# Optimization experiments

Measured on AMD Instinct MI355X. Metric: run time of the kernel, lower is better.

Reference implementation:

```python
import jax, jax.numpy as jnp
import numpy as np

C, N, B = 16, 65536, 4096  # cases, points per case, batch of case IDs


def _w(key, fan_in, fan_out):
    return jax.random.normal(key, (fan_in, fan_out), dtype=jnp.float32) / np.sqrt(fan_in).astype(np.float32)


def setup_inputs() -> dict:
    key = jax.random.key(0)
    ks = jax.random.split(key, 8)
    pts = jax.random.normal(ks[0], (C, N, 3), dtype=jnp.float32)
    inp = {
        "pts": pts,
        "W1_0": _w(ks[1], 3, 64), "b1_0": jnp.zeros((64,), jnp.float32),
        "W1_1": _w(ks[2], 64, 128), "b1_1": jnp.zeros((128,), jnp.float32),
        "W1_2": _w(ks[3], 128, 512), "b1_2": jnp.zeros((512,), jnp.float32),
        "W2_0": _w(ks[4], 512, 256), "b2_0": jnp.zeros((256,), jnp.float32),
        "W2_1": _w(ks[5], 256, 512), "b2_1": jnp.zeros((512,), jnp.float32),
        "x": jax.random.randint(ks[6], (B,), 0, C, dtype=jnp.int64),
    }
    return inp


def reference(pts, W1_0, b1_0, W1_1, b1_1, W1_2, b1_2, W2_0, b2_0, W2_1, b2_1, x):
    def mlp1(h):  # shared per-point MLP, SiLU after every layer
        h = jax.nn.silu(h @ W1_0 + b1_0)
        h = jax.nn.silu(h @ W1_1 + b1_1)
        h = jax.nn.silu(h @ W1_2 + b1_2)
        return h

    feats = mlp1(pts)                       # [C, N, F1]
    idx = jnp.argmax(feats, axis=1)         # [C, F1] critical-point indices per feature
    # gather critical points (detached in the torch original)
    fixed = jax.lax.stop_gradient(pts[jnp.arange(pts.shape[0])[:, None], idx])  # [C, F1, 3]

    feats2 = mlp1(fixed)                    # [C, F1, F1]
    latent0 = jnp.max(feats2, axis=1)       # [C, F1]

    h = jax.nn.silu(latent0 @ W2_0 + b2_0)  # [C, 256]
    latent = h @ W2_1 + b2_1                # [C, total_modes*ge_features]

    caseID_unit = jax.nn.one_hot(x, latent.shape[0], dtype=latent.dtype)  # [B, C]
    return caseID_unit @ latent             # [B, 512]
```

## Files before the change

kernel.cpp:

```cpp
#include <hip/hip_runtime.h>
#include <math.h>

#define NCASES   16
#define NPTS_BIG 65536
#define OUT_B    4096

typedef __attribute__((ext_vector_type(8))) short  short8;
typedef __attribute__((ext_vector_type(4))) float  floatx4;

__device__ __forceinline__ float silu_f(float x) {
    return x * __builtin_amdgcn_rcpf(1.0f + __expf(-x));
}

__device__ __forceinline__ unsigned f2bf_hi(float x) {
    unsigned u = __float_as_uint(x);
    return u + 0x7FFFu + ((u >> 16) & 1u);
}
__device__ __forceinline__ unsigned short f2bf(float x) {
    return (unsigned short)(f2bf_hi(x) >> 16);
}
__device__ __forceinline__ unsigned pk2bf_rtz(float lo, float hi) {
    return __builtin_amdgcn_perm(__float_as_uint(hi), __float_as_uint(lo), 0x07060302u);
}

__device__ __forceinline__ unsigned enc_f(float x) {
    unsigned u = __float_as_uint(x);
    return (u & 0x80000000u) ? ~u : (u | 0x80000000u);
}

__device__ __forceinline__ float sgpr_f(float x) {
    return __uint_as_float(__builtin_amdgcn_readfirstlane(__float_as_uint(x)));
}

__global__ void k_prep(const float* __restrict__ W11, const float* __restrict__ W12,
                       unsigned short* __restrict__ BbWs, unsigned short* __restrict__ BcWs,
                       unsigned long long* __restrict__ argBuf)
{
    int i = blockIdx.x * 256 + threadIdx.x;
    if (i < 8192) argBuf[i] = 0ull;
    {
        int j = i & 7, l = (i >> 3) & 63, t = i >> 9;
        int KT = t & 3, NT = (t >> 2) & 3, w = t >> 4;
        int k = KT * 32 + (l >> 4) * 8 + j;
        int f = w * 64 + NT * 16 + (l & 15);
        BcWs[i] = f2bf(W12[(size_t)k * 512 + f]);
    }
    if (i < 8192) {
        int j = i & 7, l = (i >> 3) & 63, t = i >> 9;
        int KT = t & 1, w = t >> 1;
        int k = KT * 32 + (l >> 4) * 8 + j;
        int f = w * 16 + (l & 15);
        BbWs[i] = f2bf(W11[(size_t)k * 128 + f]);
    }
}

template<bool GATHER>
__device__ __forceinline__ void mlp1_pipeline(
    const float* __restrict__ cpts,
    const unsigned long long* __restrict__ gIdx,
    int chunk0, int nChunks,
    const float* __restrict__ W10, const float* __restrict__ b10,
    const float* __restrict__ b11,
    const unsigned short* __restrict__ BbWs,
    const unsigned short* __restrict__ BcWs,
    unsigned short* __restrict__ s_h0,
    unsigned short* __restrict__ s_h1,
    int wf, int l, int lm, int q, float* bestv)
{
    float wA0[8], wA1[8], wA2[8], bA[8];
    #pragma unroll
    for (int j = 0; j < 8; ++j) {
        wA0[j] = sgpr_f(W10[  0 + wf * 8 + j]);
        wA1[j] = sgpr_f(W10[ 64 + wf * 8 + j]);
        wA2[j] = sgpr_f(W10[128 + wf * 8 + j]);
        bA[j]  = sgpr_f(b10[       wf * 8 + j]);
    }

    short8 Bc[16];
    #pragma unroll
    for (int t = 0; t < 16; ++t)
        Bc[t] = *(const short8*)(BcWs + (size_t)((wf * 16 + t) * 64 + l) * 8);
    short8 Bb0 = *(const short8*)(BbWs + (size_t)((wf * 2 + 0) * 64 + l) * 8);
    short8 Bb1 = *(const short8*)(BbWs + (size_t)((wf * 2 + 1) * 64 + l) * 8);

    const float bias11 = b11[wf * 16 + lm];
    const floatx4 bias4 = {bias11, bias11, bias11, bias11};
    const floatx4 fzero = {0.f, 0.f, 0.f, 0.f};

    #pragma unroll
    for (int NT = 0; NT < 4; ++NT) bestv[NT] = -INFINITY;

    float ax[2], ay[2], az[2];
    {
        const int pb = chunk0 * 128;
        #pragma unroll
        for (int h = 0; h < 2; ++h) {
            const float* sp;
            if (GATHER) {
                unsigned gi = ~(unsigned)(gIdx[pb + h * 64 + l] & 0xFFFFFFFFull);
                sp = cpts + (size_t)gi * 3;
            } else {
                sp = cpts + (size_t)(pb + h * 64 + l) * 3;
            }
            ax[h] = sp[0]; ay[h] = sp[1]; az[h] = sp[2];
        }
    }

    for (int ch = 0; ch < nChunks; ++ch) {
        #pragma unroll
        for (int h = 0; h < 2; ++h) {
            float v[8];
            #pragma unroll
            for (int j = 0; j < 8; ++j) {
                float t = fmaf(az[h], wA2[j], bA[j]);
                t = fmaf(ay[h], wA1[j], t);
                t = fmaf(ax[h], wA0[j], t);
                v[j] = silu_f(t);
            }
            uint4 hv = { pk2bf_rtz(v[0], v[1]), pk2bf_rtz(v[2], v[3]),
                         pk2bf_rtz(v[4], v[5]), pk2bf_rtz(v[6], v[7]) };
            *(uint4*)&s_h0[(h * 64 + l) * 72 + wf * 8] = hv;
        }
        __syncthreads();

        if (ch + 1 < nChunks) {
            const int pb = (chunk0 + ch + 1) * 128;
            #pragma unroll
            for (int h = 0; h < 2; ++h) {
                const float* sp;
                if (GATHER) {
                    unsigned gi = ~(unsigned)(gIdx[pb + h * 64 + l] & 0xFFFFFFFFull);
                    sp = cpts + (size_t)gi * 3;
                } else {
                    sp = cpts + (size_t)(pb + h * 64 + l) * 3;
                }
                ax[h] = sp[0]; ay[h] = sp[1]; az[h] = sp[2];
            }
        }

        #pragma unroll
        for (int MT = 0; MT < 8; ++MT) {
            const unsigned short* ar = s_h0 + (MT * 16 + lm) * 72;
            short8 a0 = *(const short8*)(ar + q * 8);
            short8 a1 = *(const short8*)(ar + 32 + q * 8);
            floatx4 acc = __builtin_amdgcn_mfma_f32_16x16x32_bf16(a0, Bb0, bias4, 0, 0, 0);
            acc = __builtin_amdgcn_mfma_f32_16x16x32_bf16(a1, Bb1, acc, 0, 0, 0);
            #pragma unroll
            for (int r = 0; r < 4; ++r) {
                unsigned uv = __float_as_uint(silu_f(acc[r]));
                s_h1[(MT * 16 + q * 4 + r) * 136 + wf * 16 + lm] = (unsigned short)(uv >> 16);
            }
        }
        __syncthreads();

        #pragma unroll
        for (int MT = 0; MT < 8; ++MT) {
            const unsigned short* ar = s_h1 + (MT * 16 + lm) * 136;
            short8 a[4];
            #pragma unroll
            for (int KT = 0; KT < 4; ++KT)
                a[KT] = *(const short8*)(ar + KT * 32 + q * 8);
            const int cbM = 127 - (ch << 5) - (MT << 2);
            #pragma unroll
            for (int NT = 0; NT < 4; ++NT) {
                floatx4 acc = __builtin_amdgcn_mfma_f32_16x16x32_bf16(a[0], Bc[NT * 4], fzero, 0, 0, 0);
                #pragma unroll
                for (int KT = 1; KT < 4; ++KT)
                    acc = __builtin_amdgcn_mfma_f32_16x16x32_bf16(a[KT], Bc[NT * 4 + KT], acc, 0, 0, 0);
                float x0 = __uint_as_float((__float_as_uint(acc[0]) & 0xFFFFFF80u) | (unsigned)(cbM));
                float x1 = __uint_as_float((__float_as_uint(acc[1]) & 0xFFFFFF80u) | (unsigned)(cbM - 1));
                float x2 = __uint_as_float((__float_as_uint(acc[2]) & 0xFFFFFF80u) | (unsigned)(cbM - 2));
                float x3 = __uint_as_float((__float_as_uint(acc[3]) & 0xFFFFFF80u) | (unsigned)(cbM - 3));
                float t0 = fmaxf(fmaxf(x0, x1), x2);
                bestv[NT] = fmaxf(fmaxf(t0, x3), bestv[NT]);
            }
        }
    }
}

__global__ __launch_bounds__(512, 4)
void k_mlp1_argmax(const float* __restrict__ pts,
                   const float* __restrict__ W10, const float* __restrict__ b10,
                   const float* __restrict__ b11, const float* __restrict__ b12,
                   const unsigned short* __restrict__ BbWs,
                   const unsigned short* __restrict__ BcWs,
                   unsigned long long* __restrict__ argOut)
{
    const int c = blockIdx.y, tid = threadIdx.x;
    const int wf = __builtin_amdgcn_readfirstlane(tid >> 6);
    const int l = tid & 63, lm = l & 15, q = l >> 4;

    __shared__ __align__(16) unsigned short s_h0[128 * 72];
    __shared__ __align__(16) unsigned short s_h1[128 * 136];

    float bestv[4];
    mlp1_pipeline<false>(pts + (size_t)c * NPTS_BIG * 3, nullptr,
                         blockIdx.x * 4, 4, W10, b10, b11, BbWs, BcWs,
                         s_h0, s_h1, wf, l, lm, q, bestv);

    #pragma unroll
    for (int NT = 0; NT < 4; ++NT) {
        unsigned u = __float_as_uint(bestv[NT]);
        int t = 127 - (int)(u & 127u);
        unsigned idx = (unsigned)((blockIdx.x * 4 + (t >> 5)) * 128
                                  + ((t >> 2) & 7) * 16 + q * 4 + (t & 3));
        float v = __uint_as_float(u & 0xFFFFFF80u) + b12[wf * 64 + NT * 16 + lm];
        #pragma unroll
        for (int m = 16; m <= 32; m <<= 1) {
            float    vo = __shfl_xor(v, m, 64);
            unsigned io = __shfl_xor(idx, m, 64);
            if (vo > v || (vo == v && io < idx)) { v = vo; idx = io; }
        }
        if (q == 0) {
            unsigned long long key = ((unsigned long long)enc_f(v) << 32)
                                   | (unsigned long long)(~idx);
            atomicMax(&argOut[(size_t)c * 512 + wf * 64 + NT * 16 + lm], key);
        }
    }
}

__global__ __launch_bounds__(512, 4)
void k_tail(const float* __restrict__ pts,
            const unsigned long long* __restrict__ argBuf,
            const float* __restrict__ W10, const float* __restrict__ b10,
            const float* __restrict__ b11, const float* __restrict__ b12,
            const unsigned short* __restrict__ BbWs,
            const unsigned short* __restrict__ BcWs,
            const float* __restrict__ W20, const float* __restrict__ b20,
            const float* __restrict__ W21, const float* __restrict__ b21,
            float* __restrict__ latent)
{
    const int c = blockIdx.x, tid = threadIdx.x;
    const int wf = __builtin_amdgcn_readfirstlane(tid >> 6);
    const int l = tid & 63, lm = l & 15, q = l >> 4;

    __shared__ __align__(16) unsigned short s_h0[128 * 72];
    __shared__ __align__(16) unsigned short s_h1[128 * 136];
    __shared__ float l0[512];
    __shared__ float red[512];
    __shared__ float hh[256];

    float bestv[4];
    mlp1_pipeline<true>(pts + (size_t)c * NPTS_BIG * 3, argBuf + (size_t)c * 512,
                        0, 4, W10, b10, b11, BbWs, BcWs,
                        s_h0, s_h1, wf, l, lm, q, bestv);

    #pragma unroll
    for (int NT = 0; NT < 4; ++NT) {
        float v = __uint_as_float(__float_as_uint(bestv[NT]) & 0xFFFFFF80u)
                + b12[wf * 64 + NT * 16 + lm];
        v = fmaxf(v, __shfl_xor(v, 16, 64));
        v = fmaxf(v, __shfl_xor(v, 32, 64));
        if (q == 0) l0[wf * 64 + NT * 16 + lm] = silu_f(v);
    }
    __syncthreads();

    {
        const int f = tid & 255, s = tid >> 8;
        float acc = 0.f;
        #pragma unroll 8
        for (int k = s * 256; k < s * 256 + 256; ++k)
            acc = fmaf(l0[k], W20[(size_t)k * 256 + f], acc);
        red[s * 256 + f] = acc;
    }
    __syncthreads();
    if (tid < 256) hh[tid] = silu_f(red[tid] + red[256 + tid] + b20[tid]);
    __syncthreads();

    {
        float acc = 0.f;
        #pragma unroll 8
        for (int k = 0; k < 256; ++k)
            acc = fmaf(hh[k], W21[(size_t)k * 512 + tid], acc);
        latent[(size_t)c * 512 + tid] = acc + b21[tid];
    }
}

__global__ void k_scatter(const int* __restrict__ x,
                          const float* __restrict__ latent,
                          float* __restrict__ out)
{
    const int b = blockIdx.x, t = threadIdx.x;
    int cid = x[b];
    const float4* src = (const float4*)(latent + (size_t)cid * 512);
    float4* dst = (float4*)(out + (size_t)b * 512);
    dst[t] = src[t];
}

extern "C" void kernel_launch(void* const* d_in, const int* in_sizes, int n_in,
                              void* d_out, int out_size, void* d_ws, size_t ws_size,
                              hipStream_t stream)
{
    const float* pts = (const float*)d_in[0];
    const float* W10 = (const float*)d_in[1];
    const float* b10 = (const float*)d_in[2];
    const float* W11 = (const float*)d_in[3];
    const float* b11 = (const float*)d_in[4];
    const float* W12 = (const float*)d_in[5];
    const float* b12 = (const float*)d_in[6];
    const float* W20 = (const float*)d_in[7];
    const float* b20 = (const float*)d_in[8];
    const float* W21 = (const float*)d_in[9];
    const float* b21 = (const float*)d_in[10];
    const int*   x   = (const int*)d_in[11];
    float* out = (float*)d_out;

    char* ws = (char*)d_ws;
    unsigned long long* argBuf = (unsigned long long*)ws;
    float* latent              = (float*)(ws + 65536);
    unsigned short* BbWs       = (unsigned short*)(ws + 98304);
    unsigned short* BcWs       = (unsigned short*)(ws + 114688);

    k_prep<<<dim3(256), dim3(256), 0, stream>>>(W11, W12, BbWs, BcWs, argBuf);

    k_mlp1_argmax<<<dim3(128, NCASES), dim3(512), 0, stream>>>(
        pts, W10, b10, b11, b12, BbWs, BcWs, argBuf);

    k_tail<<<dim3(NCASES), dim3(512), 0, stream>>>(
        pts, argBuf, W10, b10, b11, b12, BbWs, BcWs, W20, b20, W21, b21, latent);

    k_scatter<<<dim3(OUT_B), dim3(128), 0, stream>>>(x, latent, out);
}
```

Before: 279.9 us.

## Fuse case-ID scatter into tail kernel and split FMA accumulators

Removes the separate scatter kernel launch and the latent workspace round trip. Each of the 16 tail blocks now scans all 4096 case IDs with a ballot and writes its 512-float latent row to every matching output row. The two small dense layers in the tail also use four independent accumulators to break the serial FMA dependency chain. This cuts one launch and its global read of latent, but the output writes are now spread over only 16 blocks rather than 4096, which may underuse the GPU's bandwidth.

```diff
diff --git a/kernel.cpp b/kernel.cpp
--- a/kernel.cpp
+++ b/kernel.cpp
@@ -228,7 +228,7 @@
             const unsigned short* __restrict__ BcWs,
             const float* __restrict__ W20, const float* __restrict__ b20,
             const float* __restrict__ W21, const float* __restrict__ b21,
-            float* __restrict__ latent)
+            const int* __restrict__ x, float* __restrict__ out)
 {
     const int c = blockIdx.x, tid = threadIdx.x;
     const int wf = __builtin_amdgcn_readfirstlane(tid >> 6);
@@ -257,34 +257,52 @@
 
     {
         const int f = tid & 255, s = tid >> 8;
-        float acc = 0.f;
+        const float* Wp = W20 + (size_t)(s * 256) * 256 + f;
+        const float* lp = l0 + s * 256;
+        float a0 = 0.f, a1 = 0.f, a2 = 0.f, a3 = 0.f;
         #pragma unroll 8
-        for (int k = s * 256; k < s * 256 + 256; ++k)
-            acc = fmaf(l0[k], W20[(size_t)k * 256 + f], acc);
-        red[s * 256 + f] = acc;
+        for (int k = 0; k < 256; k += 4) {
+            a0 = fmaf(lp[k],     Wp[(size_t)k * 256],       a0);
+            a1 = fmaf(lp[k + 1], Wp[(size_t)(k + 1) * 256], a1);
+            a2 = fmaf(lp[k + 2], Wp[(size_t)(k + 2) * 256], a2);
+            a3 = fmaf(lp[k + 3], Wp[(size_t)(k + 3) * 256], a3);
+        }
+        red[s * 256 + f] = (a0 + a1) + (a2 + a3);
     }
     __syncthreads();
     if (tid < 256) hh[tid] = silu_f(red[tid] + red[256 + tid] + b20[tid]);
     __syncthreads();
 
     {
-        float acc = 0.f;
+        const float* Wp = W21 + tid;
+        float a0 = 0.f, a1 = 0.f, a2 = 0.f, a3 = 0.f;
         #pragma unroll 8
-        for (int k = 0; k < 256; ++k)
-            acc = fmaf(hh[k], W21[(size_t)k * 512 + tid], acc);
-        latent[(size_t)c * 512 + tid] = acc + b21[tid];
-    }
-}
-
-__global__ void k_scatter(const int* __restrict__ x,
-                          const float* __restrict__ latent,
-                          float* __restrict__ out)
-{
-    const int b = blockIdx.x, t = threadIdx.x;
-    int cid = x[b];
-    const float4* src = (const float4*)(latent + (size_t)cid * 512);
-    float4* dst = (float4*)(out + (size_t)b * 512);
-    dst[t] = src[t];
+        for (int k = 0; k < 256; k += 4) {
+            a0 = fmaf(hh[k],     Wp[(size_t)k * 512],       a0);
+            a1 = fmaf(hh[k + 1], Wp[(size_t)(k + 1) * 512], a1);
+            a2 = fmaf(hh[k + 2], Wp[(size_t)(k + 2) * 512], a2);
+            a3 = fmaf(hh[k + 3], Wp[(size_t)(k + 3) * 512], a3);
+        }
+        red[tid] = (a0 + a1) + (a2 + a3) + b21[tid];
+    }
+    __syncthreads();
+
+    {
+        float4 r0 = *(float4*)&red[l * 8];
+        float4 r1 = *(float4*)&red[l * 8 + 4];
+        #pragma unroll 1
+        for (int i = 0; i < 8; ++i) {
+            const int b = wf * 512 + i * 64 + l;
+            unsigned long long mask = __ballot(x[b] == c);
+            while (mask) {
+                int s = __ffsll((long long)mask) - 1;
+                mask &= mask - 1;
+                const int bb = wf * 512 + i * 64 + s;
+                float4* dst = (float4*)(out + (size_t)bb * 512 + l * 8);
+                dst[0] = r0; dst[1] = r1;
+            }
+        }
+    }
 }
 
 extern "C" void kernel_launch(void* const* d_in, const int* in_sizes, int n_in,
@@ -307,9 +325,8 @@
 
     char* ws = (char*)d_ws;
     unsigned long long* argBuf = (unsigned long long*)ws;
-    float* latent              = (float*)(ws + 65536);
-    unsigned short* BbWs       = (unsigned short*)(ws + 98304);
-    unsigned short* BcWs       = (unsigned short*)(ws + 114688);
+    unsigned short* BbWs       = (unsigned short*)(ws + 65536);
+    unsigned short* BcWs       = (unsigned short*)(ws + 81920);
 
     k_prep<<<dim3(256), dim3(256), 0, stream>>>(W11, W12, BbWs, BcWs, argBuf);
 
@@ -317,7 +334,5 @@
         pts, W10, b10, b11, b12, BbWs, BcWs, argBuf);
 
     k_tail<<<dim3(NCASES), dim3(512), 0, stream>>>(
-        pts, argBuf, W10, b10, b11, b12, BbWs, BcWs, W20, b20, W21, b21, latent);
-
-    k_scatter<<<dim3(OUT_B), dim3(128), 0, stream>>>(x, latent, out);
-}
+        pts, argBuf, W10, b10, b11, b12, BbWs, BcWs, W20, b20, W21, b21, x, out);
+}
```

After: 269.1 us. 1.04x faster.
